# Kernel tuning notes

Hardware: AMD Instinct MI355X
Metric: run time of the kernel (lower is better)

The kernel has to match this reference:

```python
import jax, jax.numpy as jnp
import numpy as np

N = 50000
E = 800000
IN_C = 16
H = 64
EA = 3
L = 3
EPS = 1e-5

def layer_norm(h, g, b):
    mu = jnp.mean(h, axis=-1, keepdims=True)
    var = jnp.var(h, axis=-1, keepdims=True)
    return (h - mu) * jax.lax.rsqrt(var + EPS) * g + b

def setup_inputs() -> dict:
    key = jax.random.key(0)
    ks = jax.random.split(key, 24)
    s = lambda *sh: 0.05
    d = {}
    d["x"] = jax.random.normal(ks[0], (N, IN_C), jnp.float32)
    d["edge_index"] = jax.random.randint(ks[1], (2, E), 0, N, jnp.int32)
    d["edge_attr"] = jax.random.normal(ks[2], (E, EA), jnp.float32)
    # encoder
    d["enc_w"] = jax.random.normal(ks[3], (IN_C, H), jnp.float32) * 0.1
    d["enc_b"] = jnp.zeros((H,), jnp.float32)
    d["enc_ln_g"] = jnp.ones((H,), jnp.float32)
    d["enc_ln_b"] = jnp.zeros((H,), jnp.float32)
    # message-passing MLPs (stacked over layers)
    d["mlp_w1"] = jax.random.normal(ks[4], (L, H + EA, H // 2), jnp.float32) * 0.1
    d["mlp_b1"] = jnp.zeros((L, H // 2), jnp.float32)
    d["mlp_w2"] = jax.random.normal(ks[5], (L, H // 2, H), jnp.float32) * 0.1
    d["mlp_b2"] = jnp.zeros((L, H), jnp.float32)
    d["ln_g"] = jnp.ones((L, H), jnp.float32)
    d["ln_b"] = jnp.zeros((L, H), jnp.float32)
    # heads
    d["depth_w1"] = jax.random.normal(ks[6], (H, H // 2), jnp.float32) * 0.1
    d["depth_b1"] = jnp.zeros((H // 2,), jnp.float32)
    d["depth_w2"] = jax.random.normal(ks[7], (H // 2, 1), jnp.float32) * 0.1
    d["depth_b2"] = jnp.zeros((1,), jnp.float32)
    d["vel_w1"] = jax.random.normal(ks[8], (H, H // 2), jnp.float32) * 0.1
    d["vel_b1"] = jnp.zeros((H // 2,), jnp.float32)
    d["vel_w2"] = jax.random.normal(ks[9], (H // 2, 2), jnp.float32) * 0.1
    d["vel_b2"] = jnp.zeros((2,), jnp.float32)
    return d

def reference(x, edge_index, edge_attr, enc_w, enc_b, enc_ln_g, enc_ln_b,
              mlp_w1, mlp_b1, mlp_w2, mlp_b2, ln_g, ln_b,
              depth_w1, depth_b1, depth_w2, depth_b2,
              vel_w1, vel_b1, vel_w2, vel_b2):
    src, dst = edge_index[0], edge_index[1]  # PyG: x_j = x[src], aggregate at dst
    # encoder (dropout inactive in eval mode)
    h = layer_norm(x @ enc_w + enc_b, enc_ln_g, enc_ln_b)
    h = jax.nn.relu(h)
    # in-degree counts for mean aggregation (isolated nodes -> 0, like PyG)
    cnt = jax.ops.segment_sum(jnp.ones((E,), jnp.float32), dst, num_segments=N)
    inv_cnt = jnp.where(cnt > 0, 1.0 / jnp.maximum(cnt, 1.0), 0.0)[:, None]
    for i in range(L):
        m_in = jnp.concatenate([h[src], edge_attr], axis=1)          # [E, H+EA]
        m = jax.nn.relu(m_in @ mlp_w1[i] + mlp_b1[i]) @ mlp_w2[i] + mlp_b2[i]  # [E, H]
        agg = jax.ops.segment_sum(m, dst, num_segments=N) * inv_cnt  # mean aggregate
        h = layer_norm(h + agg, ln_g[i], ln_b[i])
    depth = jax.nn.relu(h @ depth_w1 + depth_b1) @ depth_w2 + depth_b2    # [N,1]
    velocity = jax.nn.relu(h @ vel_w1 + vel_b1) @ vel_w2 + vel_b2         # [N,2]
    return (depth, velocity)
```

## Files before the change

kernel.cpp:

```cpp
#include <hip/hip_runtime.h>
#include <hip/hip_bf16.h>
#include <hip/hip_fp16.h>

typedef __hip_bfloat16 bf16;
typedef unsigned int u32;
typedef unsigned int u2v __attribute__((ext_vector_type(2)));

#define NN 50000
#define NE 800000
#define INC 16
#define HD 64
#define EPSV 1e-5f
#define NB1 196
#define CNTB 3125
#define ENCB 6250

__device__ __forceinline__ float b2f(bf16 v) { return __bfloat162float(v); }
__device__ __forceinline__ bool is_bf(const void* det) {
  return *(const u32*)det == 0x3F803F80u;
}

__device__ __forceinline__ uint2 ldnt2(const uint2* p) {
  u2v t = __builtin_nontemporal_load(reinterpret_cast<const u2v*>(p));
  uint2 r; r.x = t[0]; r.y = t[1];
  return r;
}

template<typename T> __device__ __forceinline__ float ldv(const T* p, int i);
template<> __device__ __forceinline__ float ldv<float>(const float* p, int i) { return p[i]; }
template<> __device__ __forceinline__ float ldv<bf16>(const bf16* p, int i) { return b2f(p[i]); }

#define W1F   0
#define B1F   6432
#define W2F   6528
#define B2F   12672
#define DW1F  12864
#define DB1F  14912
#define DW2F  14944
#define DB2F  14976
#define VW1F  14977
#define VB1F  17025
#define VW2F  17057
#define VB2F  17121
#define WFTOT 17123

#define H_OFF    0
#define P0_OFF   3200000
#define CSR_OFF  4800000
#define WF_OFF   8000000
#define CNTI_OFF (WF_OFF + WFTOT)
#define RS_OFF   (CNTI_OFF + NN)
#define BSUM_OFF (RS_OFF + NN)
#define BOFF_OFF (BSUM_OFF + 256)
#define LPOS_OFF (BOFF_OFF + 256)
#define INV_OFF  (LPOS_OFF + NE)
#define P1_OFF   (INV_OFF + NE)
#define WS_NEED_ROOMY ((size_t)(P1_OFF + NN * 16) * 4)

template<typename T>
__device__ __forceinline__ void prep_body(
    const T* w1, const T* b1, const T* w2, const T* b2,
    const T* dw1, const T* db1, const T* dw2, const T* db2,
    const T* vw1, const T* vb1, const T* vw2, const T* vb2,
    float* wf, int i) {
  float v;
  if      (i < B1F)  v = ldv(w1,  i - W1F);
  else if (i < W2F)  v = ldv(b1,  i - B1F);
  else if (i < B2F)  v = ldv(w2,  i - W2F);
  else if (i < DW1F) v = ldv(b2,  i - B2F);
  else if (i < DB1F) v = ldv(dw1, i - DW1F);
  else if (i < DW2F) v = ldv(db1, i - DB1F);
  else if (i < DB2F) v = ldv(dw2, i - DW2F);
  else if (i < VW1F) v = ldv(db2, i - DB2F);
  else if (i < VB1F) v = ldv(vw1, i - VW1F);
  else if (i < VW2F) v = ldv(vb1, i - VB1F);
  else if (i < VB2F) v = ldv(vw2, i - VW2F);
  else               v = ldv(vb2, i - VB2F);
  wf[i] = v;
}

__global__ __launch_bounds__(256) void prep_kernel(
    const void* w1, const void* b1, const void* w2, const void* b2,
    const void* dw1, const void* db1, const void* dw2, const void* db2,
    const void* vw1, const void* vb1, const void* vw2, const void* vb2,
    float* __restrict__ wf, const void* __restrict__ det) {
  int i = blockIdx.x * blockDim.x + threadIdx.x;
  if (i >= WFTOT) return;
  if (is_bf(det))
    prep_body((const bf16*)w1, (const bf16*)b1, (const bf16*)w2, (const bf16*)b2,
              (const bf16*)dw1, (const bf16*)db1, (const bf16*)dw2, (const bf16*)db2,
              (const bf16*)vw1, (const bf16*)vb1, (const bf16*)vw2, (const bf16*)vb2, wf, i);
  else
    prep_body((const float*)w1, (const float*)b1, (const float*)w2, (const float*)b2,
              (const float*)dw1, (const float*)db1, (const float*)dw2, (const float*)db2,
              (const float*)vw1, (const float*)vb1, (const float*)vw2, (const float*)vb2, wf, i);
}

__global__ __launch_bounds__(256) void enc_count_kernel(
    const void* __restrict__ x, const void* __restrict__ enc_w,
    const void* __restrict__ enc_b, const void* __restrict__ g,
    const void* __restrict__ b, float* __restrict__ h,
    __half* __restrict__ pout, const float* __restrict__ nw1,
    const float* __restrict__ nb1, const int* __restrict__ ei,
    int* __restrict__ cnt, int* __restrict__ lpos,
    const void* __restrict__ det) {
  if (blockIdx.x < CNTB) {
    int e = blockIdx.x * 256 + threadIdx.x;
    if (e < NE) lpos[e] = atomicAdd(&cnt[ei[NE + e]], 1);
    return;
  }
  __shared__ float shv[4][2][64];
  int wid = ((blockIdx.x - CNTB) * blockDim.x + threadIdx.x) >> 6;
  int lane = threadIdx.x & 63;
  int w = threadIdx.x >> 6;
  int n0 = 2 * wid, n1 = n0 + 1;
  if (n0 >= NN) return;
  int jl = lane & 31, half = lane >> 5;
  float xv0[INC], xv1[INC], wv[INC], ebv, gv, bv;
  if (is_bf(det)) {
    const bf16* xp0 = (const bf16*)x + n0 * INC;
    const bf16* xp1 = (const bf16*)x + n1 * INC;
    const bf16* wp = (const bf16*)enc_w;
    #pragma unroll
    for (int k = 0; k < INC; k++) {
      xv0[k] = b2f(xp0[k]); xv1[k] = b2f(xp1[k]); wv[k] = b2f(wp[k * HD + lane]);
    }
    ebv = b2f(((const bf16*)enc_b)[lane]);
    gv  = b2f(((const bf16*)g)[lane]);
    bv  = b2f(((const bf16*)b)[lane]);
  } else {
    const float* xp0 = (const float*)x + n0 * INC;
    const float* xp1 = (const float*)x + n1 * INC;
    const float* wp = (const float*)enc_w;
    #pragma unroll
    for (int k = 0; k < INC; k++) {
      xv0[k] = xp0[k]; xv1[k] = xp1[k]; wv[k] = wp[k * HD + lane];
    }
    ebv = ((const float*)enc_b)[lane];
    gv  = ((const float*)g)[lane];
    bv  = ((const float*)b)[lane];
  }
  float acc0 = ebv, acc1 = ebv;
  #pragma unroll
  for (int k = 0; k < INC; k++) { acc0 += xv0[k] * wv[k]; acc1 += xv1[k] * wv[k]; }
  float s10 = acc0, s20 = acc0 * acc0, s11 = acc1, s21 = acc1 * acc1;
  #pragma unroll
  for (int o = 32; o; o >>= 1) {
    s10 += __shfl_xor(s10, o); s20 += __shfl_xor(s20, o);
    s11 += __shfl_xor(s11, o); s21 += __shfl_xor(s21, o);
  }
  float mu0 = s10 * (1.0f / 64.0f), mu1 = s11 * (1.0f / 64.0f);
  float var0 = fmaxf(s20 * (1.0f / 64.0f) - mu0 * mu0, 0.0f);
  float var1 = fmaxf(s21 * (1.0f / 64.0f) - mu1 * mu1, 0.0f);
  float hv0 = fmaxf((acc0 - mu0) * rsqrtf(var0 + EPSV) * gv + bv, 0.0f);
  float hv1 = fmaxf((acc1 - mu1) * rsqrtf(var1 + EPSV) * gv + bv, 0.0f);
  h[n0 * HD + lane] = hv0;
  h[n1 * HD + lane] = hv1;
  shv[w][0][lane] = hv0;
  shv[w][1][lane] = hv1;
  float pacc0 = 0.0f, pacc1 = 0.0f;
  int kb = half << 5;
  #pragma unroll
  for (int k4 = 0; k4 < 32; k4 += 4) {
    float4 h0 = *reinterpret_cast<const float4*>(&shv[w][0][kb + k4]);
    float4 h1 = *reinterpret_cast<const float4*>(&shv[w][1][kb + k4]);
    int kk = kb + k4;
    float n0v = nw1[kk * 32 + jl],       n1v = nw1[(kk + 1) * 32 + jl];
    float n2v = nw1[(kk + 2) * 32 + jl], n3v = nw1[(kk + 3) * 32 + jl];
    pacc0 += h0.x * n0v + h0.y * n1v + h0.z * n2v + h0.w * n3v;
    pacc1 += h1.x * n0v + h1.y * n1v + h1.z * n2v + h1.w * n3v;
  }
  pacc0 += __shfl_xor(pacc0, 32);
  pacc1 += __shfl_xor(pacc1, 32);
  if (half == 0) {
    pout[n0 * 32 + jl] = __float2half(pacc0 + nb1[jl]);
    pout[n1 * 32 + jl] = __float2half(pacc1 + nb1[jl]);
  }
}

__global__ __launch_bounds__(256) void scan1_kernel(const int* __restrict__ cnt,
                                                    int* __restrict__ ex,
                                                    int* __restrict__ bsum) {
  __shared__ int s[256];
  int t = threadIdx.x, idx = blockIdx.x * 256 + t;
  int v = (idx < NN) ? cnt[idx] : 0;
  s[t] = v;
  __syncthreads();
  #pragma unroll
  for (int off = 1; off < 256; off <<= 1) {
    int u = (t >= off) ? s[t - off] : 0;
    __syncthreads();
    s[t] += u;
    __syncthreads();
  }
  if (idx < NN) ex[idx] = s[t] - v;
  if (t == 255) bsum[blockIdx.x] = s[255];
}

__global__ __launch_bounds__(256) void scan2_kernel(int* __restrict__ bsum,
                                                    int* __restrict__ boff) {
  __shared__ int s[256];
  int t = threadIdx.x;
  int v = (t < NB1) ? bsum[t] : 0;
  s[t] = v;
  __syncthreads();
  #pragma unroll
  for (int off = 1; off < 256; off <<= 1) {
    int u = (t >= off) ? s[t - off] : 0;
    __syncthreads();
    s[t] += u;
    __syncthreads();
  }
  boff[t] = s[t] - v;
}

__global__ __launch_bounds__(256) void scan3_kernel(int* __restrict__ rs,
                                                    const int* __restrict__ boff) {
  int idx = blockIdx.x * 256 + threadIdx.x;
  if (idx >= NN) return;
  rs[idx] += boff[blockIdx.x];
}

__global__ __launch_bounds__(256) void inv_kernel(const int* __restrict__ ei,
                                                  const int* __restrict__ rs,
                                                  const int* __restrict__ lpos,
                                                  int* __restrict__ inv) {
  int e = blockIdx.x * blockDim.x + threadIdx.x;
  if (e >= NE) return;
  int dst = ei[NE + e];
  inv[rs[dst] + lpos[e]] = e;
}

__global__ __launch_bounds__(256) void fill_kernel(const int* __restrict__ inv,
                                                   const int* __restrict__ ei,
                                                   const void* __restrict__ attr,
                                                   uint2* __restrict__ csr,
                                                   const void* __restrict__ det) {
  int p = blockIdx.x * blockDim.x + threadIdx.x;
  if (p >= NE) return;
  int e = inv[p];
  u32 src = (u32)ei[e];
  float a0, a1, a2;
  if (is_bf(det)) {
    const bf16* ap = (const bf16*)attr + 3 * e;
    a0 = b2f(ap[0]); a1 = b2f(ap[1]); a2 = b2f(ap[2]);
  } else {
    const float* ap = (const float*)attr + 3 * e;
    a0 = ap[0]; a1 = ap[1]; a2 = ap[2];
  }
  u32 lo = ((u32)__half_as_ushort(__float2half(a1)) << 16)
         | (u32)__half_as_ushort(__float2half(a0));
  u32 hi = (src << 16) | (u32)__half_as_ushort(__float2half(a2));
  uint2 v; v.x = lo; v.y = hi;
  csr[p] = v;
}

__global__ __launch_bounds__(256) void node_pre_kernel(
    const float* __restrict__ h, const float* __restrict__ w1,
    const float* __restrict__ b1, __half* __restrict__ p) {
  int t = blockIdx.x * blockDim.x + threadIdx.x;
  int node = t >> 5;
  int j = t & 31;
  if (node >= NN) return;
  const float* hr = h + node * HD;
  float acc = b1[j];
  #pragma unroll
  for (int k = 0; k < HD; k++) acc += hr[k] * w1[k * 32 + j];
  p[node * 32 + j] = __float2half(acc);
}

__global__ __launch_bounds__(128) void gather_kernel(
    float* __restrict__ h, const __half2* __restrict__ pin,
    __half* __restrict__ pnext, const uint2* __restrict__ csr,
    const int* __restrict__ rs, const int* __restrict__ cnt,
    const float* __restrict__ w1a, const float* __restrict__ w2,
    const float* __restrict__ b2v, const void* __restrict__ gbase,
    const void* __restrict__ bbase, int layer,
    const float* __restrict__ nw1, const float* __restrict__ nb1,
    int do_pnext, const float* __restrict__ wf, void* __restrict__ out,
    const void* __restrict__ det) {
  __shared__ float sacc[2][2][32];
  __shared__ float shv[2][2][64];
  int wid = (blockIdx.x * blockDim.x + threadIdx.x) >> 6;
  int lane = threadIdx.x & 63;
  int w = threadIdx.x >> 6;
  int n0 = 2 * wid, n1 = 2 * wid + 1;
  if (n0 >= NN) return;
  int jl = lane & 31, half = lane >> 5;
  int q4 = lane >> 4, pp = lane & 15;
  float2 wa0 = *reinterpret_cast<const float2*>(&w1a[2 * pp]);
  float2 wa1 = *reinterpret_cast<const float2*>(&w1a[32 + 2 * pp]);
  float2 wa2 = *reinterpret_cast<const float2*>(&w1a[64 + 2 * pp]);
  int s0 = rs[n0], c0 = cnt[n0];
  int s1 = rs[n1], c1 = cnt[n1];
  float hres0 = h[n0 * HD + lane];
  float hres1 = h[n1 * HD + lane];
  float b2l = b2v[lane];

  bool isbf = is_bf(det);
  int gidx = layer * HD + lane;
  float gv, bv;
  if (isbf) {
    gv = b2f(((const bf16*)gbase)[gidx]);
    bv = b2f(((const bf16*)bbase)[gidx]);
  } else {
    gv = ((const float*)gbase)[gidx];
    bv = ((const float*)bbase)[gidx];
  }

  int cm10 = (c0 > 0) ? c0 - 1 : 0;
  int cm11 = (c1 > 0) ? c1 - 1 : 0;
  int t0 = (c0 > 0) ? s0 : 0;
  int t1 = (c1 > 0) ? s1 : 0;

  float2 acc0 = make_float2(0.f, 0.f), acc1 = make_float2(0.f, 0.f);
  int cmax = max(c0, c1);
  if (cmax > 0) {
    uint2 e0[4], e1[4];
    #pragma unroll
    for (int t = 0; t < 4; t++) {
      e0[t] = ldnt2(&csr[t0 + min(4 * t + q4, cm10)]);
      e1[t] = ldnt2(&csr[t1 + min(4 * t + q4, cm11)]);
    }
    for (int b0 = 0; b0 < cmax; b0 += 16) {
      float2 g0[4], g1[4];
      #pragma unroll
      for (int t = 0; t < 4; t++)
        g0[t] = __half22float2(pin[(e0[t].y >> 16) * 16 + pp]);
      #pragma unroll
      for (int t = 0; t < 4; t++)
        g1[t] = __half22float2(pin[(e1[t].y >> 16) * 16 + pp]);
      float2 pa0[4], pa1[4];
      #pragma unroll
      for (int t = 0; t < 4; t++) {
        float2 a01 = __half22float2(*reinterpret_cast<const __half2*>(&e0[t].x));
        float a2 = __half2float(__ushort_as_half((unsigned short)(e0[t].y & 0xFFFFu)));
        pa0[t].x = a01.x * wa0.x + a01.y * wa1.x + a2 * wa2.x;
        pa0[t].y = a01.x * wa0.y + a01.y * wa1.y + a2 * wa2.y;
        float2 b01 = __half22float2(*reinterpret_cast<const __half2*>(&e1[t].x));
        float b2 = __half2float(__ushort_as_half((unsigned short)(e1[t].y & 0xFFFFu)));
        pa1[t].x = b01.x * wa0.x + b01.y * wa1.x + b2 * wa2.x;
        pa1[t].y = b01.x * wa0.y + b01.y * wa1.y + b2 * wa2.y;
      }
      int nb = b0 + 16;
      if (nb < cmax) {
        #pragma unroll
        for (int t = 0; t < 4; t++) {
          e0[t] = ldnt2(&csr[t0 + min(nb + 4 * t + q4, cm10)]);
          e1[t] = ldnt2(&csr[t1 + min(nb + 4 * t + q4, cm11)]);
        }
      }
      #pragma unroll
      for (int t = 0; t < 4; t++) {
        int eo = b0 + 4 * t + q4;
        float rx0 = fmaxf(g0[t].x + pa0[t].x, 0.0f);
        float ry0 = fmaxf(g0[t].y + pa0[t].y, 0.0f);
        acc0.x += (eo < c0) ? rx0 : 0.0f;
        acc0.y += (eo < c0) ? ry0 : 0.0f;
        float rx1 = fmaxf(g1[t].x + pa1[t].x, 0.0f);
        float ry1 = fmaxf(g1[t].y + pa1[t].y, 0.0f);
        acc1.x += (eo < c1) ? rx1 : 0.0f;
        acc1.y += (eo < c1) ? ry1 : 0.0f;
      }
    }
  }
  acc0.x += __shfl_xor(acc0.x, 16); acc0.y += __shfl_xor(acc0.y, 16);
  acc1.x += __shfl_xor(acc1.x, 16); acc1.y += __shfl_xor(acc1.y, 16);
  acc0.x += __shfl_xor(acc0.x, 32); acc0.y += __shfl_xor(acc0.y, 32);
  acc1.x += __shfl_xor(acc1.x, 32); acc1.y += __shfl_xor(acc1.y, 32);
  if (lane < 16) {
    *reinterpret_cast<float2*>(&sacc[w][0][2 * pp]) = acc0;
    *reinterpret_cast<float2*>(&sacc[w][1][2 * pp]) = acc1;
  }

  float m0 = 0.0f, m1 = 0.0f;
  #pragma unroll
  for (int j4 = 0; j4 < 32; j4 += 4) {
    float4 a0 = *reinterpret_cast<const float4*>(&sacc[w][0][j4]);
    float4 a1 = *reinterpret_cast<const float4*>(&sacc[w][1][j4]);
    float w20 = w2[(j4 + 0) * HD + lane], w21 = w2[(j4 + 1) * HD + lane];
    float w22 = w2[(j4 + 2) * HD + lane], w23 = w2[(j4 + 3) * HD + lane];
    m0 += a0.x * w20 + a0.y * w21 + a0.z * w22 + a0.w * w23;
    m1 += a1.x * w20 + a1.y * w21 + a1.z * w22 + a1.w * w23;
  }
  float aggv0 = (c0 > 0) ? (m0 / (float)c0 + b2l) : 0.0f;
  float aggv1 = (c1 > 0) ? (m1 / (float)c1 + b2l) : 0.0f;

  float v0 = hres0 + aggv0, v1 = hres1 + aggv1;
  float s10 = v0, s20 = v0 * v0, s11 = v1, s21 = v1 * v1;
  #pragma unroll
  for (int o = 32; o; o >>= 1) {
    s10 += __shfl_xor(s10, o); s20 += __shfl_xor(s20, o);
    s11 += __shfl_xor(s11, o); s21 += __shfl_xor(s21, o);
  }
  float mu0 = s10 * (1.0f / 64.0f), mu1 = s11 * (1.0f / 64.0f);
  float var0 = fmaxf(s20 * (1.0f / 64.0f) - mu0 * mu0, 0.0f);
  float var1 = fmaxf(s21 * (1.0f / 64.0f) - mu1 * mu1, 0.0f);
  float hv0 = (v0 - mu0) * rsqrtf(var0 + EPSV) * gv + bv;
  float hv1 = (v1 - mu1) * rsqrtf(var1 + EPSV) * gv + bv;

  shv[w][0][lane] = hv0;
  shv[w][1][lane] = hv1;

  if (do_pnext) {
    float p0a = 0.0f, p1a = 0.0f;
    int kb = half << 5;
    #pragma unroll
    for (int k4 = 0; k4 < 32; k4 += 4) {
      float4 h0 = *reinterpret_cast<const float4*>(&shv[w][0][kb + k4]);
      float4 h1 = *reinterpret_cast<const float4*>(&shv[w][1][kb + k4]);
      int kk = kb + k4;
      float n0v = nw1[kk * 32 + jl], n1v = nw1[(kk + 1) * 32 + jl];
      float n2v = nw1[(kk + 2) * 32 + jl], n3v = nw1[(kk + 3) * 32 + jl];
      p0a += h0.x * n0v + h0.y * n1v + h0.z * n2v + h0.w * n3v;
      p1a += h1.x * n0v + h1.y * n1v + h1.z * n2v + h1.w * n3v;
    }
    p0a += __shfl_xor(p0a, 32);
    p1a += __shfl_xor(p1a, 32);
    if (half == 0) {
      pnext[n0 * 32 + jl] = __float2half(p0a + nb1[jl]);
      pnext[n1 * 32 + jl] = __float2half(p1a + nb1[jl]);
    }
  }

  if (layer == 2) {
    const float* w1h = wf + (half ? VW1F : DW1F);
    float a20 = half ? wf[VB1F + jl] : wf[DB1F + jl];
    float a21 = a20;
    #pragma unroll
    for (int k4 = 0; k4 < 64; k4 += 4) {
      float4 h0 = *reinterpret_cast<const float4*>(&shv[w][0][k4]);
      float4 h1 = *reinterpret_cast<const float4*>(&shv[w][1][k4]);
      float wv0 = w1h[(k4 + 0) * 32 + jl], wv1 = w1h[(k4 + 1) * 32 + jl];
      float wv2 = w1h[(k4 + 2) * 32 + jl], wv3 = w1h[(k4 + 3) * 32 + jl];
      a20 += h0.x * wv0 + h0.y * wv1 + h0.z * wv2 + h0.w * wv3;
      a21 += h1.x * wv0 + h1.y * wv1 + h1.z * wv2 + h1.w * wv3;
    }
    a20 = fmaxf(a20, 0.0f);
    a21 = fmaxf(a21, 0.0f);
    float r00, r10, r01, r11;
    if (half == 0) {
      r00 = a20 * wf[DW2F + jl]; r10 = 0.0f;
      r01 = a21 * wf[DW2F + jl]; r11 = 0.0f;
    } else {
      r00 = a20 * wf[VW2F + 2 * jl]; r10 = a20 * wf[VW2F + 2 * jl + 1];
      r01 = a21 * wf[VW2F + 2 * jl]; r11 = a21 * wf[VW2F + 2 * jl + 1];
    }
    #pragma unroll
    for (int o = 16; o; o >>= 1) {
      r00 += __shfl_xor(r00, o); r10 += __shfl_xor(r10, o);
      r01 += __shfl_xor(r01, o); r11 += __shfl_xor(r11, o);
    }
    if (lane == 0) {
      float d0 = r00 + wf[DB2F];
      float d1 = r01 + wf[DB2F];
      if (isbf) {
        ((bf16*)out)[n0] = __float2bfloat16(d0);
        ((bf16*)out)[n1] = __float2bfloat16(d1);
      } else {
        ((float*)out)[n0] = d0;
        ((float*)out)[n1] = d1;
      }
    }
    if (lane == 32) {
      float v00 = r00 + wf[VB2F], v01 = r10 + wf[VB2F + 1];
      float v10 = r01 + wf[VB2F], v11 = r11 + wf[VB2F + 1];
      if (isbf) {
        ((bf16*)out)[NN + 2 * n0]     = __float2bfloat16(v00);
        ((bf16*)out)[NN + 2 * n0 + 1] = __float2bfloat16(v01);
        ((bf16*)out)[NN + 2 * n1]     = __float2bfloat16(v10);
        ((bf16*)out)[NN + 2 * n1 + 1] = __float2bfloat16(v11);
      } else {
        ((float*)out)[NN + 2 * n0]     = v00;
        ((float*)out)[NN + 2 * n0 + 1] = v01;
        ((float*)out)[NN + 2 * n1]     = v10;
        ((float*)out)[NN + 2 * n1 + 1] = v11;
      }
    }
  } else {
    h[n0 * HD + lane] = hv0;
    h[n1 * HD + lane] = hv1;
  }
}

extern "C" void kernel_launch(void* const* d_in, const int* in_sizes, int n_in,
                              void* d_out, int out_size, void* d_ws, size_t ws_size,
                              hipStream_t stream) {
  const void* x     = d_in[0];
  const int*  ei    = (const int*)d_in[1];
  const void* attr  = d_in[2];
  const void* enc_w = d_in[3];
  const void* enc_b = d_in[4];
  const void* enc_g = d_in[5];
  const void* enc_bb= d_in[6];
  const void* mw1   = d_in[7];
  const void* mb1   = d_in[8];
  const void* mw2   = d_in[9];
  const void* mb2   = d_in[10];
  const void* lng   = d_in[11];
  const void* lnb   = d_in[12];
  const void* dw1   = d_in[13];
  const void* db1   = d_in[14];
  const void* dw2   = d_in[15];
  const void* db2   = d_in[16];
  const void* vw1   = d_in[17];
  const void* vb1   = d_in[18];
  const void* vw2   = d_in[19];
  const void* vb2   = d_in[20];

  float* ws    = (float*)d_ws;
  float* h     = ws + H_OFF;
  __half* p0   = (__half*)(ws + P0_OFF);
  uint2* csr   = (uint2*)(ws + CSR_OFF);
  float* wf    = ws + WF_OFF;
  int*   cnti  = (int*)(ws + CNTI_OFF);
  int*   rs    = (int*)(ws + RS_OFF);
  int*   bsum  = (int*)(ws + BSUM_OFF);
  int*   boff  = (int*)(ws + BOFF_OFF);
  int*   lpos  = (int*)(ws + LPOS_OFF);
  int*   inv   = (int*)(ws + INV_OFF);
  __half* p1   = (__half*)(ws + P1_OFF);
  bool roomy = ws_size >= WS_NEED_ROOMY;

  hipMemsetAsync(cnti, 0, (size_t)NN * sizeof(int), stream);
  prep_kernel<<<(WFTOT + 255) / 256, 256, 0, stream>>>(
      mw1, mb1, mw2, mb2, dw1, db1, dw2, db2, vw1, vb1, vw2, vb2, wf, enc_g);
  enc_count_kernel<<<CNTB + ENCB, 256, 0, stream>>>(
      x, enc_w, enc_b, enc_g, enc_bb, h, p0, wf + W1F, wf + B1F,
      ei, cnti, lpos, enc_g);
  scan1_kernel<<<NB1, 256, 0, stream>>>(cnti, rs, bsum);
  scan2_kernel<<<1, 256, 0, stream>>>(bsum, boff);
  scan3_kernel<<<NB1, 256, 0, stream>>>(rs, boff);
  inv_kernel<<<(NE + 255) / 256, 256, 0, stream>>>(ei, rs, lpos, inv);
  fill_kernel<<<(NE + 255) / 256, 256, 0, stream>>>(inv, ei, attr, csr, enc_g);

  for (int l = 0; l < 3; l++) {
    __half* pin  = (roomy && (l & 1)) ? p1 : p0;
    __half* pnxt = (roomy && !(l & 1)) ? p1 : p0;
    if (!roomy && l > 0) {
      node_pre_kernel<<<(NN * 32 + 255) / 256, 256, 0, stream>>>(
          h, wf + W1F + l * 2144, wf + B1F + l * 32, p0);
      pin = p0; pnxt = p0;
    }
    int do_pnext = (roomy && l < 2) ? 1 : 0;
    int nl = (l < 2) ? l + 1 : l;
    gather_kernel<<<(NN + 3) / 4, 128, 0, stream>>>(
        h, (const __half2*)pin, pnxt, csr, rs, cnti,
        wf + W1F + l * 2144 + 64 * 32, wf + W2F + l * 2048, wf + B2F + l * 64,
        lng, lnb, l,
        wf + W1F + nl * 2144, wf + B1F + nl * 32, do_pnext,
        wf, d_out, enc_g);
  }
}
```

Baseline: 330.6 us.

## Sort nodes by in-degree descending to balance gather wavefront work

Builds a 64-bin degree histogram during the scan and a counting-sort permutation that orders nodes by descending in-degree. The gather kernel then handles nodes in permuted order, so each wavefront's two nodes have similar edge counts and heavy nodes are scheduled first. This targets load imbalance and idle lanes across the degree distribution. The cost is an extra kernel, atomics, and a perm lookup, and node h/p accesses become scattered rather than contiguous, which may hurt memory locality.

```diff
diff --git a/kernel.cpp b/kernel.cpp
--- a/kernel.cpp
+++ b/kernel.cpp
@@ -14,6 +14,7 @@
 #define NB1 196
 #define CNTB 3125
 #define ENCB 6250
+#define NBIN 64
 
 __device__ __forceinline__ float b2f(bf16 v) { return __bfloat162float(v); }
 __device__ __forceinline__ bool is_bf(const void* det) {
@@ -49,12 +50,15 @@
 #define CSR_OFF  4800000
 #define WF_OFF   8000000
 #define CNTI_OFF (WF_OFF + WFTOT)
-#define RS_OFF   (CNTI_OFF + NN)
+#define DH_OFF   (CNTI_OFF + NN)
+#define DC_OFF   (DH_OFF + NBIN)
+#define RS_OFF   (DC_OFF + NBIN)
 #define BSUM_OFF (RS_OFF + NN)
 #define BOFF_OFF (BSUM_OFF + 256)
 #define LPOS_OFF (BOFF_OFF + 256)
 #define INV_OFF  (LPOS_OFF + NE)
-#define P1_OFF   (INV_OFF + NE)
+#define PERM_OFF (INV_OFF + NE)
+#define P1_OFF   (PERM_OFF + NN)
 #define WS_NEED_ROOMY ((size_t)(P1_OFF + NN * 16) * 4)
 
 template<typename T>
@@ -180,11 +184,16 @@
 
 __global__ __launch_bounds__(256) void scan1_kernel(const int* __restrict__ cnt,
                                                     int* __restrict__ ex,
-                                                    int* __restrict__ bsum) {
+                                                    int* __restrict__ bsum,
+                                                    int* __restrict__ dhist) {
   __shared__ int s[256];
   int t = threadIdx.x, idx = blockIdx.x * 256 + t;
   int v = (idx < NN) ? cnt[idx] : 0;
   s[t] = v;
+  if (idx < NN) {
+    int bin = (NBIN - 1) - min(v, NBIN - 1);
+    atomicAdd(&dhist[bin], 1);
+  }
   __syncthreads();
   #pragma unroll
   for (int off = 1; off < 256; off <<= 1) {
@@ -198,11 +207,15 @@
 }
 
 __global__ __launch_bounds__(256) void scan2_kernel(int* __restrict__ bsum,
-                                                    int* __restrict__ boff) {
+                                                    int* __restrict__ boff,
+                                                    int* __restrict__ dhist) {
   __shared__ int s[256];
+  __shared__ int d[NBIN];
   int t = threadIdx.x;
   int v = (t < NB1) ? bsum[t] : 0;
   s[t] = v;
+  int dv = 0;
+  if (t < NBIN) { dv = dhist[t]; d[t] = dv; }
   __syncthreads();
   #pragma unroll
   for (int off = 1; off < 256; off <<= 1) {
@@ -212,6 +225,14 @@
     __syncthreads();
   }
   boff[t] = s[t] - v;
+  #pragma unroll
+  for (int off = 1; off < NBIN; off <<= 1) {
+    int u = (t >= off && t < NBIN) ? d[t - off] : 0;
+    __syncthreads();
+    if (t < NBIN) d[t] += u;
+    __syncthreads();
+  }
+  if (t < NBIN) dhist[t] = d[t] - dv;
 }
 
 __global__ __launch_bounds__(256) void scan3_kernel(int* __restrict__ rs,
@@ -219,6 +240,17 @@
   int idx = blockIdx.x * 256 + threadIdx.x;
   if (idx >= NN) return;
   rs[idx] += boff[blockIdx.x];
+}
+
+__global__ __launch_bounds__(256) void perm_kernel(const int* __restrict__ cnt,
+                                                   const int* __restrict__ dbase,
+                                                   int* __restrict__ dcur,
+                                                   int* __restrict__ perm) {
+  int idx = blockIdx.x * 256 + threadIdx.x;
+  if (idx >= NN) return;
+  int bin = (NBIN - 1) - min(cnt[idx], NBIN - 1);
+  int pos = dbase[bin] + atomicAdd(&dcur[bin], 1);
+  perm[pos] = idx;
 }
 
 __global__ __launch_bounds__(256) void inv_kernel(const int* __restrict__ ei,
@@ -273,6 +305,7 @@
     float* __restrict__ h, const __half2* __restrict__ pin,
     __half* __restrict__ pnext, const uint2* __restrict__ csr,
     const int* __restrict__ rs, const int* __restrict__ cnt,
+    const int* __restrict__ perm,
     const float* __restrict__ w1a, const float* __restrict__ w2,
     const float* __restrict__ b2v, const void* __restrict__ gbase,
     const void* __restrict__ bbase, int layer,
@@ -284,8 +317,8 @@
   int wid = (blockIdx.x * blockDim.x + threadIdx.x) >> 6;
   int lane = threadIdx.x & 63;
   int w = threadIdx.x >> 6;
-  int n0 = 2 * wid, n1 = 2 * wid + 1;
-  if (n0 >= NN) return;
+  if (2 * wid >= NN) return;
+  int n0 = perm[2 * wid], n1 = perm[2 * wid + 1];
   int jl = lane & 31, half = lane >> 5;
   int q4 = lane >> 4, pp = lane & 15;
   float2 wa0 = *reinterpret_cast<const float2*>(&w1a[2 * pp]);
@@ -514,23 +547,27 @@
   uint2* csr   = (uint2*)(ws + CSR_OFF);
   float* wf    = ws + WF_OFF;
   int*   cnti  = (int*)(ws + CNTI_OFF);
+  int*   dhist = (int*)(ws + DH_OFF);
+  int*   dcur  = (int*)(ws + DC_OFF);
   int*   rs    = (int*)(ws + RS_OFF);
   int*   bsum  = (int*)(ws + BSUM_OFF);
   int*   boff  = (int*)(ws + BOFF_OFF);
   int*   lpos  = (int*)(ws + LPOS_OFF);
   int*   inv   = (int*)(ws + INV_OFF);
+  int*   perm  = (int*)(ws + PERM_OFF);
   __half* p1   = (__half*)(ws + P1_OFF);
   bool roomy = ws_size >= WS_NEED_ROOMY;
 
-  hipMemsetAsync(cnti, 0, (size_t)NN * sizeof(int), stream);
+  hipMemsetAsync(cnti, 0, (size_t)(NN + 2 * NBIN) * sizeof(int), stream);
   prep_kernel<<<(WFTOT + 255) / 256, 256, 0, stream>>>(
       mw1, mb1, mw2, mb2, dw1, db1, dw2, db2, vw1, vb1, vw2, vb2, wf, enc_g);
   enc_count_kernel<<<CNTB + ENCB, 256, 0, stream>>>(
       x, enc_w, enc_b, enc_g, enc_bb, h, p0, wf + W1F, wf + B1F,
       ei, cnti, lpos, enc_g);
-  scan1_kernel<<<NB1, 256, 0, stream>>>(cnti, rs, bsum);
-  scan2_kernel<<<1, 256, 0, stream>>>(bsum, boff);
+  scan1_kernel<<<NB1, 256, 0, stream>>>(cnti, rs, bsum, dhist);
+  scan2_kernel<<<1, 256, 0, stream>>>(bsum, boff, dhist);
   scan3_kernel<<<NB1, 256, 0, stream>>>(rs, boff);
+  perm_kernel<<<NB1, 256, 0, stream>>>(cnti, dhist, dcur, perm);
   inv_kernel<<<(NE + 255) / 256, 256, 0, stream>>>(ei, rs, lpos, inv);
   fill_kernel<<<(NE + 255) / 256, 256, 0, stream>>>(inv, ei, attr, csr, enc_g);
 
@@ -545,7 +582,7 @@
     int do_pnext = (roomy && l < 2) ? 1 : 0;
     int nl = (l < 2) ? l + 1 : l;
     gather_kernel<<<(NN + 3) / 4, 128, 0, stream>>>(
-        h, (const __half2*)pin, pnxt, csr, rs, cnti,
+        h, (const __half2*)pin, pnxt, csr, rs, cnti, perm,
         wf + W1F + l * 2144 + 64 * 32, wf + W2F + l * 2048, wf + B2F + l * 64,
         lng, lnb, l,
         wf + W1F + nl * 2144, wf + B1F + nl * 32, do_pnext,
```

Measured after the change: 604.0 us. 1.83x slower.
